# Optimization experiments

Measured on AMD Instinct MI355X. Metric: run time of the kernel, lower is better.

The kernel has to match this reference:

```python
import jax, jax.numpy as jnp
import numpy as np

B, C, H, W = 64, 256, 64, 64
E = 4                      # num_experts
CELL = 8
OUT = CELL * CELL + 1      # 65
EPS_BN = 1e-5
EPS_LB = 1e-6


def setup_inputs() -> dict:
    key = jax.random.key(0)
    ks = jax.random.split(key, 6)
    x = jax.random.normal(ks[0], (B, C, H, W), dtype=jnp.float32)
    w_experts = jax.random.normal(ks[1], (E, C, OUT), dtype=jnp.float32) * 0.05
    b_experts = jax.random.normal(ks[2], (E, OUT), dtype=jnp.float32) * 0.05
    w_gate = jax.random.normal(ks[3], (C, E), dtype=jnp.float32) * 0.05
    b_gate = jax.random.normal(ks[4], (E,), dtype=jnp.float32) * 0.05
    gamma = jnp.ones((OUT,), dtype=jnp.float32)
    beta = jnp.zeros((OUT,), dtype=jnp.float32)
    return {"x": x, "w_experts": w_experts, "b_experts": b_experts,
            "w_gate": w_gate, "b_gate": b_gate, "gamma": gamma, "beta": beta}


def pixel_shuffle(t, r):
    n, ch, h, w = t.shape
    nc = ch // (r * r)
    t = t.reshape(n, nc, r, r, h, w)
    t = t.transpose(0, 1, 4, 2, 5, 3)
    return t.reshape(n, nc, h * r, w * r)


def reference(x, w_experts, b_experts, w_gate, b_gate, gamma, beta):
    x = jax.nn.relu(x)
    xh = x.transpose(0, 2, 3, 1)                       # [B,H,W,C]

    # gating: global-avg-pool -> linear -> softmax -> hard top-1
    pooled = xh.mean(axis=(1, 2))                      # [B,C]
    gate = jax.nn.softmax(pooled @ w_gate + b_gate, axis=-1)
    idx = jnp.argmax(gate, axis=-1)                    # [B]

    # load-balancing KL(usage || uniform)
    usage = jnp.mean(jax.nn.one_hot(idx, E, dtype=xh.dtype), axis=0) + EPS_LB
    usage = usage / usage.sum()
    lb_loss = jnp.sum(usage * (jnp.log(usage) - jnp.log(jnp.full_like(usage, 1.0 / E))))

    # fused gather->grouped-GEMM (per-sample expert weight selection)
    w_sel = w_experts[idx]                             # [B,C,OUT]
    b_sel = b_experts[idx]                             # [B,OUT]
    y = jnp.einsum('bhwc,bco->bhwo', xh, w_sel) + b_sel[:, None, None, :]
    y = y.transpose(0, 3, 1, 2)                        # [B,OUT,H,W]

    # BatchNorm2d (training mode: batch statistics, biased variance)
    mean = y.mean(axis=(0, 2, 3), keepdims=True)
    var = y.var(axis=(0, 2, 3), keepdims=True)
    logits = (y - mean) / jnp.sqrt(var + EPS_BN)
    logits = logits * gamma[None, :, None, None] + beta[None, :, None, None]

    prob = jax.nn.softmax(logits, axis=1)[:, :-1]      # drop dustbin channel
    prob = pixel_shuffle(prob, CELL)                   # [B,1,H*8,W*8]
    prob = prob[:, 0]                                  # squeeze dim=1
    return logits, prob, lb_loss
```

## Files before the change

kernel.cpp:

```cpp
#include <hip/hip_runtime.h>
#include <stdint.h>
#include <math.h>

#define B_    64
#define C_    256
#define HW_   4096
#define E_    4
#define OUT_  65
#define NPAD_ 80

#define LOGITS_SZ (B_*OUT_*HW_)
#define PROB_SZ   (B_*512*512)

#define POOLED_OFF 0u
#define IDX_OFF    65536u
#define BNSUM_OFF  65792u
#define BNSS_OFF   66112u
#define WT_OFF     67072u
#define YB_OFF     230912u
#define CLEAR_BYTES 66432u

typedef float  f4 __attribute__((ext_vector_type(4)));
typedef short  s8 __attribute__((ext_vector_type(8)));

__device__ __forceinline__ uint32_t f2bf(float f){
  uint32_t u = __float_as_uint(f);
  return (u + 0x7FFFu + ((u >> 16) & 1u)) >> 16;
}
__device__ __forceinline__ uint32_t pk(float lo, float hi){
  return f2bf(lo) | (f2bf(hi) << 16);
}
__device__ __forceinline__ float bf2f(uint32_t u){
  return __uint_as_float((u & 0xFFFFu) << 16);
}


__global__ __launch_bounds__(256) void k_prep(const float* __restrict__ x,
                                              uint16_t* __restrict__ xb,
                                              float* __restrict__ pooled){
  __shared__ float pool_lds[64];
  int bid = blockIdx.x;
  int b = bid >> 7, ct = (bid >> 5) & 3, pt = bid & 31;
  int t = threadIdx.x;
  int cg = t & 7, pgg = t >> 3;
  int c0 = ct*64 + cg*8;
  int p0 = pt*128 + pgg*4;
  if (t < 64) pool_lds[t] = 0.f;
  __syncthreads();

  float v[8][4]; float s[8];
  const float* xp = x + ((size_t)(b*C_ + c0))*HW_ + p0;
#pragma unroll
  for (int r = 0; r < 8; ++r){
    float4 f = *(const float4*)(xp + (size_t)r*HW_);
    v[r][0]=fmaxf(f.x,0.f); v[r][1]=fmaxf(f.y,0.f);
    v[r][2]=fmaxf(f.z,0.f); v[r][3]=fmaxf(f.w,0.f);
    s[r] = v[r][0]+v[r][1]+v[r][2]+v[r][3];
  }
  int ksg  = ct*2 + (cg >> 2);
  int quad = cg & 3;
#pragma unroll
  for (int pp = 0; pp < 4; ++pp){
    int p = p0 + pp;
    uint16_t* dst = xb + ((((size_t)(b*256 + (p>>4))*8 + ksg)*64)
                          + (size_t)((p&15)*4 + quad))*8;
    uint4 w;
    w.x = pk(v[0][pp], v[1][pp]); w.y = pk(v[2][pp], v[3][pp]);
    w.z = pk(v[4][pp], v[5][pp]); w.w = pk(v[6][pp], v[7][pp]);
    *(uint4*)dst = w;
  }
#pragma unroll
  for (int r = 0; r < 8; ++r){
    float vv = s[r];
    vv += __shfl_xor(vv, 8);
    vv += __shfl_xor(vv, 16);
    vv += __shfl_xor(vv, 32);
    if ((t & 56) == 0)
      atomicAdd(&pool_lds[cg*8 + r], vv);
  }
  __syncthreads();
  if (t < 64) atomicAdd(pooled + b*C_ + ct*64 + t, pool_lds[t]);
}

__global__ void k_wtgate(const float* __restrict__ w_experts,
                         const float* __restrict__ w_gate,
                         const float* __restrict__ b_gate,
                         const float* __restrict__ pooled_sum,
                         uint16_t* __restrict__ Wt,
                         int* __restrict__ idx_ws,
                         float* __restrict__ out_lb){
  int bid = blockIdx.x;
  int t = threadIdx.x;
  if (bid < 320){
    if (t >= 32) return;
    int e = bid / NPAD_, o = bid % NPAD_;
    int ks = t >> 2, quad = t & 3;
    int c = t*8;
    float a[8];
    if (o < OUT_){
      const float* src = w_experts + (size_t)e*C_*OUT_ + o;
#pragma unroll
      for (int j = 0; j < 8; ++j) a[j] = src[(size_t)(c+j)*OUT_];
    } else {
#pragma unroll
      for (int j = 0; j < 8; ++j) a[j] = 0.f;
    }
    uint4 w;
    w.x = pk(a[0],a[1]); w.y = pk(a[2],a[3]);
    w.z = pk(a[4],a[5]); w.w = pk(a[6],a[7]);
    uint16_t* dst = Wt + ((((size_t)(e*5 + (o>>4))*8 + ks)*64)
                          + (size_t)((o&15)*4 + quad))*8;
    *(uint4*)dst = w;
    return;
  }
  __shared__ float gl[64][4];
  __shared__ int ish[64];
  int b = t >> 2, e = t & 3;
  float dot = 0.f;
  const float* pr = pooled_sum + b*C_;
  for (int c = 0; c < C_; c += 4){
    float4 p4 = *(const float4*)(pr + c);
    dot += p4.x*w_gate[c*4+e] + p4.y*w_gate[(c+1)*4+e]
         + p4.z*w_gate[(c+2)*4+e] + p4.w*w_gate[(c+3)*4+e];
  }
  gl[b][e] = dot * (1.f/4096.f) + b_gate[e];
  __syncthreads();
  if (t < 64){
    float best = gl[t][0]; int bi = 0;
    for (int ee = 1; ee < 4; ++ee){ float vv = gl[t][ee]; if (vv > best){best = vv; bi = ee;} }
    idx_ws[t] = bi; ish[t] = bi;
  }
  __syncthreads();
  if (t == 0){
    int cnt[4] = {0,0,0,0};
    for (int bb = 0; bb < 64; ++bb) cnt[ish[bb]]++;
    double u[4], S = 0.0;
    for (int ee = 0; ee < 4; ++ee){ u[ee] = cnt[ee]/64.0 + 1e-6; S += u[ee]; }
    double lb = 0.0;
    for (int ee = 0; ee < 4; ++ee){ double uu = u[ee]/S; lb += uu*(log(uu) - log(0.25)); }
    *out_lb = (float)lb;
  }
}

__global__ __launch_bounds__(256) void k_gemm(const uint16_t* __restrict__ xb,
                                              const uint16_t* __restrict__ Wt,
                                              const int* __restrict__ idx_ws,
                                              const float* __restrict__ b_experts,
                                              uint16_t* __restrict__ yb,
                                              float* __restrict__ bnsum,
                                              float* __restrict__ bnss){
  __shared__ float2 bnp[NPAD_*4];
  int bid = blockIdx.x;
  int b = bid >> 4, pt = bid & 15;
  int t = threadIdx.x;
  int w = t >> 6, lane = t & 63;
  int l15 = lane & 15, quad = lane >> 4;
  int lid = l15*4 + quad;
  int e = idx_ws[b];
  int p0 = pt*256 + w*64;
  const uint16_t* ap = xb + ((size_t)(b*256 + pt*16 + w*4))*4096 + (size_t)lid*8;
  const uint16_t* bp = Wt + (size_t)e*5*4096 + (size_t)lid*8;

  f4 acc[4][5];
#pragma unroll
  for (int mt=0; mt<4; ++mt)
#pragma unroll
    for (int nt=0; nt<5; ++nt){ f4 z = {0.f,0.f,0.f,0.f}; acc[mt][nt] = z; }

#pragma unroll
  for (int ks = 0; ks < 8; ++ks){
    s8 av[4], bv[5];
#pragma unroll
    for (int mt=0; mt<4; ++mt) av[mt] = *(const s8*)(ap + (size_t)mt*4096 + ks*512);
#pragma unroll
    for (int nt=0; nt<5; ++nt) bv[nt] = *(const s8*)(bp + (size_t)nt*4096 + ks*512);
#pragma unroll
    for (int mt=0; mt<4; ++mt)
#pragma unroll
      for (int nt=0; nt<5; ++nt)
        acc[mt][nt] = __builtin_amdgcn_mfma_f32_16x16x32_bf16(av[mt], bv[nt], acc[mt][nt], 0, 0, 0);
  }

#pragma unroll
  for (int nt=0; nt<5; ++nt){
    int o = nt*16 + l15;
    float bias = (o < OUT_) ? b_experts[e*OUT_ + o] : 0.f;
    float s1 = 0.f, s2 = 0.f;
#pragma unroll
    for (int mt=0; mt<4; ++mt){
#pragma unroll
      for (int r=0; r<4; ++r){
        float vv = acc[mt][nt][r] + bias;
        acc[mt][nt][r] = vv;
        s1 += vv; s2 += vv*vv;
      }
      if (o < OUT_){
        size_t base = ((size_t)(b*OUT_ + o))*HW_ + p0 + mt*16 + quad*4;
        uint2 st;
        st.x = pk(acc[mt][nt][0], acc[mt][nt][1]);
        st.y = pk(acc[mt][nt][2], acc[mt][nt][3]);
        *(uint2*)(yb + base) = st;
      }
    }
    s1 += __shfl_xor(s1, 16); s1 += __shfl_xor(s1, 32);
    s2 += __shfl_xor(s2, 16); s2 += __shfl_xor(s2, 32);
    if (quad == 0) bnp[(nt*16 + l15)*4 + w] = make_float2(s1, s2);
  }
  __syncthreads();
  if (t < OUT_){
    float2 a0 = bnp[t*4+0], a1 = bnp[t*4+1], a2 = bnp[t*4+2], a3 = bnp[t*4+3];
    atomicAdd(bnsum + t, a0.x+a1.x+a2.x+a3.x);
    atomicAdd(bnss  + t, a0.y+a1.y+a2.y+a3.y);
  }
}

__global__ __launch_bounds__(256) void k_final(const uint16_t* __restrict__ yb,
                                               const float* __restrict__ bnsum,
                                               const float* __restrict__ bnss,
                                               const float* __restrict__ gamma,
                                               const float* __restrict__ beta,
                                               float* __restrict__ out_logits,
                                               float* __restrict__ out_prob){
  __shared__ float lt[OUT_*132];
  __shared__ float2 ss[OUT_];
  int bid = blockIdx.x;
  int b = bid >> 5, pt = bid & 31;
  int p0 = pt*128;
  int t = threadIdx.x;
  if (t < OUT_){
    const float invN = 1.f/(float)(B_*HW_);
    float mean = bnsum[t]*invN;
    float var  = bnss[t]*invN - mean*mean;
    float sc   = gamma[t] / sqrtf(var + 1e-5f);
    ss[t] = make_float2(sc, beta[t] - mean*sc);
  }
  __syncthreads();

  int prr = t & 15, og = t >> 4;
#pragma unroll
  for (int oi = 0; oi < 5; ++oi){
    int o = og + oi*16;
    if (o < OUT_){
      size_t base = ((size_t)(b*OUT_ + o))*HW_ + p0 + prr*8;
      uint4 raw = *(const uint4*)(yb + base);
      float f[8];
      f[0]=bf2f(raw.x); f[1]=bf2f(raw.x>>16);
      f[2]=bf2f(raw.y); f[3]=bf2f(raw.y>>16);
      f[4]=bf2f(raw.z); f[5]=bf2f(raw.z>>16);
      f[6]=bf2f(raw.w); f[7]=bf2f(raw.w>>16);
      float2 sv = ss[o];
#pragma unroll
      for (int k=0;k<8;++k) f[k] = f[k]*sv.x + sv.y;
      float4 w0 = make_float4(f[0],f[1],f[2],f[3]);
      float4 w1 = make_float4(f[4],f[5],f[6],f[7]);
      *(float4*)(out_logits + base)     = w0;
      *(float4*)(out_logits + base + 4) = w1;
      float* lp = lt + o*132 + prr*8;
      *(float4*)(lp)     = w0;
      *(float4*)(lp + 4) = w1;
    }
  }
  __syncthreads();

  if (t < 128){
    float m = -1e30f;
    for (int o = 0; o < OUT_; ++o) m = fmaxf(m, lt[o*132 + t]);
    float ssum = 0.f;
    for (int o = 0; o < OUT_; ++o) ssum += __expf(lt[o*132 + t] - m);
    float inv = 1.f/ssum;
    int P = p0 + t;
    int h = P >> 6, wd = P & 63;
    float* pb = out_prob + ((size_t)b << 18) + (size_t)(h*8)*512 + wd*8;
#pragma unroll
    for (int r1 = 0; r1 < 8; ++r1){
      float4 q0, q1;
      q0.x = __expf(lt[(r1*8+0)*132+t]-m)*inv;
      q0.y = __expf(lt[(r1*8+1)*132+t]-m)*inv;
      q0.z = __expf(lt[(r1*8+2)*132+t]-m)*inv;
      q0.w = __expf(lt[(r1*8+3)*132+t]-m)*inv;
      q1.x = __expf(lt[(r1*8+4)*132+t]-m)*inv;
      q1.y = __expf(lt[(r1*8+5)*132+t]-m)*inv;
      q1.z = __expf(lt[(r1*8+6)*132+t]-m)*inv;
      q1.w = __expf(lt[(r1*8+7)*132+t]-m)*inv;
      *(float4*)(pb + r1*512)     = q0;
      *(float4*)(pb + r1*512 + 4) = q1;
    }
  }
}

extern "C" void kernel_launch(void* const* d_in, const int* in_sizes, int n_in,
                              void* d_out, int out_size, void* d_ws, size_t ws_size,
                              hipStream_t stream){
  const float* x         = (const float*)d_in[0];
  const float* w_experts = (const float*)d_in[1];
  const float* b_experts = (const float*)d_in[2];
  const float* w_gate    = (const float*)d_in[3];
  const float* b_gate    = (const float*)d_in[4];
  const float* gamma     = (const float*)d_in[5];
  const float* beta      = (const float*)d_in[6];

  float* out = (float*)d_out;
  char*  ws  = (char*)d_ws;
  float*     pooled = (float*)(ws + POOLED_OFF);
  int*       idxw   = (int*)(ws + IDX_OFF);
  float*     bnsum  = (float*)(ws + BNSUM_OFF);
  float*     bnss   = (float*)(ws + BNSS_OFF);
  uint16_t*  Wt     = (uint16_t*)(ws + WT_OFF);
  uint16_t*  ybm    = (uint16_t*)(ws + YB_OFF);
  uint16_t*  xbm    = (uint16_t*)d_out;

  float* logits = out;
  float* prob   = out + LOGITS_SZ;
  float* lb     = out + LOGITS_SZ + PROB_SZ;

  hipMemsetAsync(ws, 0, CLEAR_BYTES, stream);
  k_prep  <<<8192, 256, 0, stream>>>(x, xbm, pooled);
  k_wtgate<<<321, 256, 0, stream>>>(w_experts, w_gate, b_gate, pooled, Wt, idxw, lb);
  k_gemm  <<<1024, 256, 0, stream>>>(xbm, Wt, idxw, b_experts, ybm, bnsum, bnss);
  k_final <<<2048, 256, 0, stream>>>(ybm, bnsum, bnss, gamma, beta, logits, prob);
}
```

Measured before the change: 499.2 us.

## Fold gating into GEMM, spread BN atomics, parallelize softmax, drop wtgate kernel

```diff
diff --git a/kernel.cpp b/kernel.cpp
--- a/kernel.cpp
+++ b/kernel.cpp
@@ -8,17 +8,17 @@
 #define E_    4
 #define OUT_  65
 #define NPAD_ 80
+#define NSPREAD_ 16
 
 #define LOGITS_SZ (B_*OUT_*HW_)
 #define PROB_SZ   (B_*512*512)
 
 #define POOLED_OFF 0u
-#define IDX_OFF    65536u
-#define BNSUM_OFF  65792u
-#define BNSS_OFF   66112u
-#define WT_OFF     67072u
-#define YB_OFF     230912u
-#define CLEAR_BYTES 66432u
+#define BNS_OFF    65536u
+#define BNSS_OFF   70656u
+#define CLEAR_BYTES 75776u
+#define WT_OFF     75776u
+#define YB_OFF     239616u
 
 typedef float  f4 __attribute__((ext_vector_type(4)));
 typedef short  s8 __attribute__((ext_vector_type(8)));
@@ -36,14 +36,41 @@
 
 
 __global__ __launch_bounds__(256) void k_prep(const float* __restrict__ x,
+                                              const float* __restrict__ w_experts,
                                               uint16_t* __restrict__ xb,
+                                              uint16_t* __restrict__ Wt,
                                               float* __restrict__ pooled){
   __shared__ float pool_lds[64];
   int bid = blockIdx.x;
+  int t = threadIdx.x;
+
+  if (bid >= 8192){
+    if (t >= 32) return;
+    int pid = bid - 8192;
+    int e = pid / NPAD_, o = pid % NPAD_;
+    int ks = t >> 2, quad = t & 3;
+    int c = t*8;
+    float a[8];
+    if (o < OUT_){
+      const float* src = w_experts + (size_t)e*C_*OUT_ + o;
+#pragma unroll
+      for (int j = 0; j < 8; ++j) a[j] = src[(size_t)(c+j)*OUT_];
+    } else {
+#pragma unroll
+      for (int j = 0; j < 8; ++j) a[j] = 0.f;
+    }
+    uint4 wv;
+    wv.x = pk(a[0],a[1]); wv.y = pk(a[2],a[3]);
+    wv.z = pk(a[4],a[5]); wv.w = pk(a[6],a[7]);
+    uint16_t* dst = Wt + ((((size_t)(e*5 + (o>>4))*8 + ks)*64)
+                          + (size_t)((o&15)*4 + quad))*8;
+    *(uint4*)dst = wv;
+    return;
+  }
+
   int b = bid >> 7, ct = (bid >> 5) & 3, pt = bid & 31;
-  int t = threadIdx.x;
-  int cg = t & 7, pgg = t >> 3;
-  int c0 = ct*64 + cg*8;
+  int cg_ = t & 7, pgg = t >> 3;
+  int c0 = ct*64 + cg_*8;
   int p0 = pt*128 + pgg*4;
   if (t < 64) pool_lds[t] = 0.f;
   __syncthreads();
@@ -57,17 +84,16 @@
     v[r][2]=fmaxf(f.z,0.f); v[r][3]=fmaxf(f.w,0.f);
     s[r] = v[r][0]+v[r][1]+v[r][2]+v[r][3];
   }
-  int ksg  = ct*2 + (cg >> 2);
-  int quad = cg & 3;
+  int ksg  = ct*2 + (cg_ >> 2);
+  int quad = cg_ & 3;
+  uint16_t* dst0 = xb + ((((size_t)(b*256 + (p0>>4))*8 + ksg)*64)
+                         + (size_t)((p0&15)*4 + quad))*8;
 #pragma unroll
   for (int pp = 0; pp < 4; ++pp){
-    int p = p0 + pp;
-    uint16_t* dst = xb + ((((size_t)(b*256 + (p>>4))*8 + ksg)*64)
-                          + (size_t)((p&15)*4 + quad))*8;
     uint4 w;
     w.x = pk(v[0][pp], v[1][pp]); w.y = pk(v[2][pp], v[3][pp]);
     w.z = pk(v[4][pp], v[5][pp]); w.w = pk(v[6][pp], v[7][pp]);
-    *(uint4*)dst = w;
+    *(uint4*)(dst0 + pp*32) = w;
   }
 #pragma unroll
   for (int r = 0; r < 8; ++r){
@@ -76,109 +102,73 @@
     vv += __shfl_xor(vv, 16);
     vv += __shfl_xor(vv, 32);
     if ((t & 56) == 0)
-      atomicAdd(&pool_lds[cg*8 + r], vv);
+      atomicAdd(&pool_lds[cg_*8 + r], vv);
   }
   __syncthreads();
   if (t < 64) atomicAdd(pooled + b*C_ + ct*64 + t, pool_lds[t]);
-}
-
-__global__ void k_wtgate(const float* __restrict__ w_experts,
-                         const float* __restrict__ w_gate,
-                         const float* __restrict__ b_gate,
-                         const float* __restrict__ pooled_sum,
-                         uint16_t* __restrict__ Wt,
-                         int* __restrict__ idx_ws,
-                         float* __restrict__ out_lb){
-  int bid = blockIdx.x;
-  int t = threadIdx.x;
-  if (bid < 320){
-    if (t >= 32) return;
-    int e = bid / NPAD_, o = bid % NPAD_;
-    int ks = t >> 2, quad = t & 3;
-    int c = t*8;
-    float a[8];
-    if (o < OUT_){
-      const float* src = w_experts + (size_t)e*C_*OUT_ + o;
-#pragma unroll
-      for (int j = 0; j < 8; ++j) a[j] = src[(size_t)(c+j)*OUT_];
-    } else {
-#pragma unroll
-      for (int j = 0; j < 8; ++j) a[j] = 0.f;
-    }
-    uint4 w;
-    w.x = pk(a[0],a[1]); w.y = pk(a[2],a[3]);
-    w.z = pk(a[4],a[5]); w.w = pk(a[6],a[7]);
-    uint16_t* dst = Wt + ((((size_t)(e*5 + (o>>4))*8 + ks)*64)
-                          + (size_t)((o&15)*4 + quad))*8;
-    *(uint4*)dst = w;
-    return;
-  }
-  __shared__ float gl[64][4];
-  __shared__ int ish[64];
-  int b = t >> 2, e = t & 3;
-  float dot = 0.f;
-  const float* pr = pooled_sum + b*C_;
-  for (int c = 0; c < C_; c += 4){
-    float4 p4 = *(const float4*)(pr + c);
-    dot += p4.x*w_gate[c*4+e] + p4.y*w_gate[(c+1)*4+e]
-         + p4.z*w_gate[(c+2)*4+e] + p4.w*w_gate[(c+3)*4+e];
-  }
-  gl[b][e] = dot * (1.f/4096.f) + b_gate[e];
-  __syncthreads();
-  if (t < 64){
-    float best = gl[t][0]; int bi = 0;
-    for (int ee = 1; ee < 4; ++ee){ float vv = gl[t][ee]; if (vv > best){best = vv; bi = ee;} }
-    idx_ws[t] = bi; ish[t] = bi;
-  }
-  __syncthreads();
-  if (t == 0){
-    int cnt[4] = {0,0,0,0};
-    for (int bb = 0; bb < 64; ++bb) cnt[ish[bb]]++;
-    double u[4], S = 0.0;
-    for (int ee = 0; ee < 4; ++ee){ u[ee] = cnt[ee]/64.0 + 1e-6; S += u[ee]; }
-    double lb = 0.0;
-    for (int ee = 0; ee < 4; ++ee){ double uu = u[ee]/S; lb += uu*(log(uu) - log(0.25)); }
-    *out_lb = (float)lb;
-  }
 }
 
 __global__ __launch_bounds__(256) void k_gemm(const uint16_t* __restrict__ xb,
                                               const uint16_t* __restrict__ Wt,
-                                              const int* __restrict__ idx_ws,
+                                              const float* __restrict__ pooled,
+                                              const float* __restrict__ w_gate,
+                                              const float* __restrict__ b_gate,
                                               const float* __restrict__ b_experts,
                                               uint16_t* __restrict__ yb,
                                               float* __restrict__ bnsum,
                                               float* __restrict__ bnss){
   __shared__ float2 bnp[NPAD_*4];
+  __shared__ float glog[4];
+  __shared__ int esh;
   int bid = blockIdx.x;
-  int b = bid >> 4, pt = bid & 15;
+  int b = bid >> 5, pt = bid & 31;
   int t = threadIdx.x;
   int w = t >> 6, lane = t & 63;
   int l15 = lane & 15, quad = lane >> 4;
   int lid = l15*4 + quad;
-  int e = idx_ws[b];
-  int p0 = pt*256 + w*64;
-  const uint16_t* ap = xb + ((size_t)(b*256 + pt*16 + w*4))*4096 + (size_t)lid*8;
+
+  if (t < 4){
+    float dot = 0.f;
+    const float* pr = pooled + b*C_;
+    for (int c = 0; c < C_; c += 4){
+      float4 p4 = *(const float4*)(pr + c);
+      dot += p4.x*w_gate[c*4+t] + p4.y*w_gate[(c+1)*4+t]
+           + p4.z*w_gate[(c+2)*4+t] + p4.w*w_gate[(c+3)*4+t];
+    }
+    glog[t] = dot * (1.f/4096.f) + b_gate[t];
+  }
+  __syncthreads();
+  if (t == 0){
+    float best = glog[0]; int bi = 0;
+#pragma unroll
+    for (int ee = 1; ee < 4; ++ee){ float vv = glog[ee]; if (vv > best){best = vv; bi = ee;} }
+    esh = bi;
+  }
+  __syncthreads();
+  int e = esh;
+
+  int p0 = pt*128 + w*32;
+  const uint16_t* ap = xb + ((size_t)(b*256 + pt*8 + w*2))*4096 + (size_t)lid*8;
   const uint16_t* bp = Wt + (size_t)e*5*4096 + (size_t)lid*8;
 
-  f4 acc[4][5];
-#pragma unroll
-  for (int mt=0; mt<4; ++mt)
+  f4 acc[2][5];
+#pragma unroll
+  for (int mt=0; mt<2; ++mt)
 #pragma unroll
     for (int nt=0; nt<5; ++nt){ f4 z = {0.f,0.f,0.f,0.f}; acc[mt][nt] = z; }
 
 #pragma unroll
   for (int ks = 0; ks < 8; ++ks){
-    s8 av[4], bv[5];
-#pragma unroll
-    for (int mt=0; mt<4; ++mt) av[mt] = *(const s8*)(ap + (size_t)mt*4096 + ks*512);
+    s8 bv[5];
 #pragma unroll
     for (int nt=0; nt<5; ++nt) bv[nt] = *(const s8*)(bp + (size_t)nt*4096 + ks*512);
 #pragma unroll
-    for (int mt=0; mt<4; ++mt)
+    for (int mt=0; mt<2; ++mt){
+      s8 av = *(const s8*)(ap + (size_t)mt*4096 + ks*512);
 #pragma unroll
       for (int nt=0; nt<5; ++nt)
-        acc[mt][nt] = __builtin_amdgcn_mfma_f32_16x16x32_bf16(av[mt], bv[nt], acc[mt][nt], 0, 0, 0);
+        acc[mt][nt] = __builtin_amdgcn_mfma_f32_16x16x32_bf16(av, bv[nt], acc[mt][nt], 0, 0, 0);
+    }
   }
 
 #pragma unroll
@@ -187,7 +177,7 @@
     float bias = (o < OUT_) ? b_experts[e*OUT_ + o] : 0.f;
     float s1 = 0.f, s2 = 0.f;
 #pragma unroll
-    for (int mt=0; mt<4; ++mt){
+    for (int mt=0; mt<2; ++mt){
 #pragma unroll
       for (int r=0; r<4; ++r){
         float vv = acc[mt][nt][r] + bias;
@@ -209,8 +199,8 @@
   __syncthreads();
   if (t < OUT_){
     float2 a0 = bnp[t*4+0], a1 = bnp[t*4+1], a2 = bnp[t*4+2], a3 = bnp[t*4+3];
-    atomicAdd(bnsum + t, a0.x+a1.x+a2.x+a3.x);
-    atomicAdd(bnss  + t, a0.y+a1.y+a2.y+a3.y);
+    atomicAdd(bnsum + (bid & (NSPREAD_-1))*NPAD_ + t, a0.x+a1.x+a2.x+a3.x);
+    atomicAdd(bnss  + (bid & (NSPREAD_-1))*NPAD_ + t, a0.y+a1.y+a2.y+a3.y);
   }
 }
 
@@ -219,18 +209,28 @@
                                                const float* __restrict__ bnss,
                                                const float* __restrict__ gamma,
                                                const float* __restrict__ beta,
+                                               const float* __restrict__ pooled,
+                                               const float* __restrict__ w_gate,
+                                               const float* __restrict__ b_gate,
                                                float* __restrict__ out_logits,
-                                               float* __restrict__ out_prob){
+                                               float* __restrict__ out_prob,
+                                               float* __restrict__ out_lb){
   __shared__ float lt[OUT_*132];
   __shared__ float2 ss[OUT_];
+  __shared__ float sden[256];
+  __shared__ float gl[64][4];
+  __shared__ int ish[64];
   int bid = blockIdx.x;
   int b = bid >> 5, pt = bid & 31;
   int p0 = pt*128;
   int t = threadIdx.x;
   if (t < OUT_){
+    float s1 = 0.f, s2 = 0.f;
+#pragma unroll
+    for (int k = 0; k < NSPREAD_; ++k){ s1 += bnsum[k*NPAD_ + t]; s2 += bnss[k*NPAD_ + t]; }
     const float invN = 1.f/(float)(B_*HW_);
-    float mean = bnsum[t]*invN;
-    float var  = bnss[t]*invN - mean*mean;
+    float mean = s1*invN;
+    float var  = s2*invN - mean*mean;
     float sc   = gamma[t] / sqrtf(var + 1e-5f);
     ss[t] = make_float2(sc, beta[t] - mean*sc);
   }
@@ -262,28 +262,67 @@
   }
   __syncthreads();
 
-  if (t < 128){
-    float m = -1e30f;
-    for (int o = 0; o < OUT_; ++o) m = fmaxf(m, lt[o*132 + t]);
+  int px = t & 127, hf = t >> 7;
+  {
+    int obeg = hf ? 33 : 0, oend = hf ? OUT_ : 33;
     float ssum = 0.f;
-    for (int o = 0; o < OUT_; ++o) ssum += __expf(lt[o*132 + t] - m);
-    float inv = 1.f/ssum;
-    int P = p0 + t;
-    int h = P >> 6, wd = P & 63;
-    float* pb = out_prob + ((size_t)b << 18) + (size_t)(h*8)*512 + wd*8;
-#pragma unroll
-    for (int r1 = 0; r1 < 8; ++r1){
+    for (int o = obeg; o < oend; ++o){
+      float ev = __expf(lt[o*132 + px]);
+      lt[o*132 + px] = ev;
+      ssum += ev;
+    }
+    sden[hf*128 + px] = ssum;
+  }
+  __syncthreads();
+  {
+    float inv = 1.f/(sden[px] + sden[128 + px]);
+    int P = p0 + px;
+    int hh = P >> 6, wd = P & 63;
+    float* pb = out_prob + ((size_t)b << 18) + (size_t)(hh*8)*512 + (size_t)wd*8;
+#pragma unroll
+    for (int r1i = 0; r1i < 4; ++r1i){
+      int r1 = hf*4 + r1i;
       float4 q0, q1;
-      q0.x = __expf(lt[(r1*8+0)*132+t]-m)*inv;
-      q0.y = __expf(lt[(r1*8+1)*132+t]-m)*inv;
-      q0.z = __expf(lt[(r1*8+2)*132+t]-m)*inv;
-      q0.w = __expf(lt[(r1*8+3)*132+t]-m)*inv;
-      q1.x = __expf(lt[(r1*8+4)*132+t]-m)*inv;
-      q1.y = __expf(lt[(r1*8+5)*132+t]-m)*inv;
-      q1.z = __expf(lt[(r1*8+6)*132+t]-m)*inv;
-      q1.w = __expf(lt[(r1*8+7)*132+t]-m)*inv;
-      *(float4*)(pb + r1*512)     = q0;
-      *(float4*)(pb + r1*512 + 4) = q1;
+      q0.x = lt[(r1*8+0)*132+px]*inv;
+      q0.y = lt[(r1*8+1)*132+px]*inv;
+      q0.z = lt[(r1*8+2)*132+px]*inv;
+      q0.w = lt[(r1*8+3)*132+px]*inv;
+      q1.x = lt[(r1*8+4)*132+px]*inv;
+      q1.y = lt[(r1*8+5)*132+px]*inv;
+      q1.z = lt[(r1*8+6)*132+px]*inv;
+      q1.w = lt[(r1*8+7)*132+px]*inv;
+      *(float4*)(pb + (size_t)r1*512)     = q0;
+      *(float4*)(pb + (size_t)r1*512 + 4) = q1;
+    }
+  }
+
+  if (bid == 0){
+    __syncthreads();
+    int bb = t >> 2, ee = t & 3;
+    float dot = 0.f;
+    const float* pr = pooled + bb*C_;
+    for (int c = 0; c < C_; c += 4){
+      float4 p4 = *(const float4*)(pr + c);
+      dot += p4.x*w_gate[c*4+ee] + p4.y*w_gate[(c+1)*4+ee]
+           + p4.z*w_gate[(c+2)*4+ee] + p4.w*w_gate[(c+3)*4+ee];
+    }
+    gl[bb][ee] = dot * (1.f/4096.f) + b_gate[ee];
+    __syncthreads();
+    if (t < 64){
+      float best = gl[t][0]; int bi = 0;
+#pragma unroll
+      for (int e2 = 1; e2 < 4; ++e2){ float vv = gl[t][e2]; if (vv > best){best = vv; bi = e2;} }
+      ish[t] = bi;
+    }
+    __syncthreads();
+    if (t == 0){
+      int cnt[4] = {0,0,0,0};
+      for (int b2 = 0; b2 < 64; ++b2) cnt[ish[b2]]++;
+      double u[4], S = 0.0;
+      for (int e2 = 0; e2 < 4; ++e2){ u[e2] = cnt[e2]/64.0 + 1e-6; S += u[e2]; }
+      double lbv = 0.0;
+      for (int e2 = 0; e2 < 4; ++e2){ double uu = u[e2]/S; lbv += uu*(log(uu) - log(0.25)); }
+      *out_lb = (float)lbv;
     }
   }
 }
@@ -302,8 +341,7 @@
   float* out = (float*)d_out;
   char*  ws  = (char*)d_ws;
   float*     pooled = (float*)(ws + POOLED_OFF);
-  int*       idxw   = (int*)(ws + IDX_OFF);
-  float*     bnsum  = (float*)(ws + BNSUM_OFF);
+  float*     bnsum  = (float*)(ws + BNS_OFF);
   float*     bnss   = (float*)(ws + BNSS_OFF);
   uint16_t*  Wt     = (uint16_t*)(ws + WT_OFF);
   uint16_t*  ybm    = (uint16_t*)(ws + YB_OFF);
@@ -311,11 +349,12 @@
 
   float* logits = out;
   float* prob   = out + LOGITS_SZ;
-  float* lb     = out + LOGITS_SZ + PROB_SZ;
+  float* lbp    = out + LOGITS_SZ + PROB_SZ;
 
   hipMemsetAsync(ws, 0, CLEAR_BYTES, stream);
-  k_prep  <<<8192, 256, 0, stream>>>(x, xbm, pooled);
-  k_wtgate<<<321, 256, 0, stream>>>(w_experts, w_gate, b_gate, pooled, Wt, idxw, lb);
-  k_gemm  <<<1024, 256, 0, stream>>>(xbm, Wt, idxw, b_experts, ybm, bnsum, bnss);
-  k_final <<<2048, 256, 0, stream>>>(ybm, bnsum, bnss, gamma, beta, logits, prob);
-}
+  k_prep <<<8512, 256, 0, stream>>>(x, w_experts, xbm, Wt, pooled);
+  k_gemm <<<2048, 256, 0, stream>>>(xbm, Wt, pooled, w_gate, b_gate, b_experts,
+                                    ybm, bnsum, bnss);
+  k_final<<<2048, 256, 0, stream>>>(ybm, bnsum, bnss, gamma, beta,
+                                    pooled, w_gate, b_gate, logits, prob, lbp);
+}
```

New measurement: 488.2 us. 1.02x faster.
